# Optimization experiments

Measured on AMD Instinct MI355X. Metric: run time of the kernel, lower is better.

Reference implementation:

```python
import jax, jax.numpy as jnp
import numpy as np

N = 30000      # node_size / new_node_size
R = 1000       # rel_size
T = 300000     # triple_size (edges)
D = 128        # node_hid == rel_hid
B = 1024       # train pairs
NNZ = 600000   # nnz of ent_adj / rel_adj
DEPTH = 2
GAMMA = 3.0
EPS = 1e-12    # F.normalize eps


def setup_inputs():
    key = jax.random.key(0)
    ks = jax.random.split(key, 12)
    adj = jnp.stack([jax.random.randint(ks[0], (T,), 0, N),
                     jax.random.randint(ks[1], (T,), 0, N)]).astype(jnp.int64)
    # one relation per triple: row ids are 0..T-1, col ids are relation ids
    r_index = jnp.stack([jnp.arange(T),
                         jax.random.randint(ks[2], (T,), 0, R)]).astype(jnp.int64)
    r_val = jnp.ones((T,), jnp.float32)
    ent_adj = jnp.stack([jax.random.randint(ks[3], (NNZ,), 0, N),
                         jax.random.randint(ks[4], (NNZ,), 0, N)]).astype(jnp.int64)
    rel_adj = jnp.stack([jax.random.randint(ks[5], (NNZ,), 0, N),
                         jax.random.randint(ks[6], (NNZ,), 0, R)]).astype(jnp.int64)
    ent_emb = jax.random.normal(ks[7], (N, D), jnp.float32) * 0.05
    rel_emb = jax.random.normal(ks[8], (R, D), jnp.float32) * 0.05
    attn_e = jax.random.normal(ks[9], (DEPTH, D, 1), jnp.float32) * 0.1
    attn_r = jax.random.normal(ks[10], (DEPTH, D, 1), jnp.float32) * 0.1
    train_pairs = jax.random.randint(ks[11], (B, 2), 0, N).astype(jnp.int64)
    return dict(ent_emb=ent_emb, rel_emb=rel_emb, attn_e=attn_e, attn_r=attn_r,
                r_val=r_val, adj=adj, r_index=r_index, ent_adj=ent_adj,
                rel_adj=rel_adj, train_pairs=train_pairs)


def _segment_softmax(vals, seg, num):
    m = jax.ops.segment_max(vals, seg, num_segments=num)
    e = jnp.exp(vals - m[seg])
    s = jax.ops.segment_sum(e, seg, num_segments=num)
    return e / s[seg]


def _avg(adj, emb):
    # sparse softmax of an all-ones matrix over dim=1 == 1/deg per nonzero, then spmm
    row, col = adj[0], adj[1]
    deg = jax.ops.segment_sum(jnp.ones_like(row, emb.dtype), row, num_segments=N)
    return jax.ops.segment_sum(emb[col] / deg[row][:, None], row, num_segments=N)


def _gat(features, rel_emb, adj, r_index, r_val, kernels):
    features = jnp.tanh(features)
    outputs = [features]
    row, col = adj[0], adj[1]
    for l in range(DEPTH):
        # sparse [T,R] @ rel_emb  -> per-triple relation embedding
        tri_rel = jax.ops.segment_sum(r_val[:, None] * rel_emb[r_index[1]],
                                      r_index[0], num_segments=T)          # [T,D]
        tri_rel = tri_rel / jnp.maximum(
            jnp.linalg.norm(tri_rel, axis=1, keepdims=True), EPS)
        neighs = features[col]                                             # [T,D]
        neighs = neighs - 2.0 * jnp.sum(neighs * tri_rel, axis=1,
                                        keepdims=True) * tri_rel
        att = jnp.squeeze(tri_rel @ kernels[l], axis=-1)                   # [T]
        att = _segment_softmax(att, row, N)
        new_features = jax.ops.segment_sum(neighs * att[:, None], row,
                                           num_segments=N)
        features = jnp.tanh(new_features)
        outputs.append(features)
    return jnp.concatenate(outputs, axis=-1)  # [N, (DEPTH+1)*D]


def _align_loss(pairs, emb):
    l, r = pairs[:, 0], pairs[:, 1]
    l_emb, r_emb = emb[l], emb[r]
    pos = jnp.sum(jnp.square(l_emb - r_emb), axis=-1, keepdims=True)       # [B,1]

    def sqdist(A, Bm):
        return (jnp.sum(jnp.square(A), axis=1)[:, None]
                + jnp.sum(jnp.square(Bm), axis=1)[None, :]
                - 2.0 * A @ Bm.T)

    bi = jnp.arange(pairs.shape[0])
    mask = jnp.ones((pairs.shape[0], N), emb.dtype)
    mask = mask.at[bi, l].add(-1.0).at[bi, r].add(-1.0)  # 1 - onehot(l) - onehot(r)

    def norm_lse(loss):
        mu = jax.lax.stop_gradient(jnp.mean(loss, axis=-1, keepdims=True))
        sd = jax.lax.stop_gradient(jnp.std(loss, axis=-1, keepdims=True))
        loss = (loss - mu) / sd
        return jax.nn.logsumexp(20.0 * loss + 8.0, axis=-1)

    l_loss = norm_lse((pos - sqdist(l_emb, emb) + GAMMA) * mask)
    r_loss = norm_lse((pos - sqdist(r_emb, emb) + GAMMA) * mask)
    return jnp.mean(l_loss + r_loss)


def reference(ent_emb, rel_emb, attn_e, attn_r, r_val, adj, r_index,
              ent_adj, rel_adj, train_pairs):
    ent_feature = _avg(ent_adj, ent_emb)   # [N,D]
    rel_feature = _avg(rel_adj, rel_emb)   # [N,D]
    out_rel = _gat(rel_feature, rel_emb, adj, r_index, r_val, attn_r)
    out_ent = _gat(ent_feature, rel_emb, adj, r_index, r_val, attn_e)
    emb = jnp.concatenate([out_ent, out_rel], axis=-1)  # [N, 6*D]
    return _align_loss(train_pairs, emb)
```

## Files before the change

### kernel.cpp

```cpp
#include <hip/hip_runtime.h>
#include <math.h>

#define N_ENT 30000
#define R_REL 1000
#define T_EDGE 300000
#define B_PAIR 1024
#define NNZ_E 600000
#define GAMMAF 3.0f
#define EPSV 1e-12f
#define EMBD 768
#define NPAD 30720
#define NT128 240
#define PTILES 480

typedef _Float16 half8 __attribute__((ext_vector_type(8)));
typedef _Float16 half4v __attribute__((ext_vector_type(4)));
typedef _Float16 half2v __attribute__((ext_vector_type(2)));
typedef float f32x4 __attribute__((ext_vector_type(4)));

__device__ inline void gl_lds16(const _Float16* g, _Float16* l){
  __builtin_amdgcn_global_load_lds(
      (const __attribute__((address_space(1))) unsigned int*)g,
      (__attribute__((address_space(3))) unsigned int*)l, 16, 0, 0);
}

__device__ inline float waveRedSum(float v){
  #pragma unroll
  for(int m=32;m>=1;m>>=1) v += __shfl_xor(v, m, 64);
  return v;
}

__device__ inline float fast_tanh(float x){
  x = fminf(10.f, fmaxf(-10.f, x));
  float e = __expf(2.f*x);
  return (e-1.f)/(e+1.f);
}

__global__ __launch_bounds__(256) void k_count3(const int* __restrict__ rA, int* cA,
                                                const int* __restrict__ rE, int* cE,
                                                const int* __restrict__ rR, int* cR){
  int e = blockIdx.x*256 + threadIdx.x;
  if(e < T_EDGE) atomicAdd(&cA[rA[e]], 1);
  if(e < NNZ_E){ atomicAdd(&cE[rE[e]], 1); atomicAdd(&cR[rR[e]], 1); }
}

__global__ __launch_bounds__(1024) void k_scan3(const int* c0, int* s0, int* u0,
                                                const int* c1, int* s1, int* u1,
                                                const int* c2, int* s2, int* u2){
  const int* cnt = blockIdx.x==0 ? c0 : (blockIdx.x==1 ? c1 : c2);
  int* start     = blockIdx.x==0 ? s0 : (blockIdx.x==1 ? s1 : s2);
  int* cursor    = blockIdx.x==0 ? u0 : (blockIdx.x==1 ? u1 : u2);
  __shared__ int wsum[16];
  __shared__ int carry;
  int tid = threadIdx.x, lane = tid & 63, wid = tid >> 6;
  if(tid==0) carry = 0;
  __syncthreads();
  for(int base=0; base<N_ENT; base+=1024){
    int i = base + tid;
    int v = (i<N_ENT)? cnt[i] : 0;
    int x = v;
    #pragma unroll
    for(int off=1; off<64; off<<=1){ int t=__shfl_up(x,off,64); if(lane>=off) x+=t; }
    if(lane==63) wsum[wid]=x;
    __syncthreads();
    if(wid==0){
      int s = (lane<16)? wsum[lane] : 0;
      #pragma unroll
      for(int off=1; off<16; off<<=1){ int t=__shfl_up(s,off,64); if(lane>=off) s+=t; }
      if(lane<16) wsum[lane]=s;
    }
    __syncthreads();
    int wexcl = (wid==0)? 0 : wsum[wid-1];
    int excl = carry + wexcl + x - v;
    if(i<N_ENT){ start[i]=excl; cursor[i]=excl; }
    int tot = wsum[15];
    __syncthreads();
    if(tid==0) carry += tot;
    __syncthreads();
  }
  if(tid==0) start[N_ENT] = carry;
}

__global__ __launch_bounds__(256) void k_scatter3(
      const int* __restrict__ rA, const int* __restrict__ cAj, const int* __restrict__ rid,
      int* uA, int* scolA, int* sridA,
      const int* __restrict__ rE, const int* __restrict__ cEj, int* uE, int* scolE,
      const int* __restrict__ rR, const int* __restrict__ cRj, int* uR, int* scolR){
  int e = blockIdx.x*256 + threadIdx.x;
  if(e < T_EDGE){
    int p = atomicAdd(&uA[rA[e]], 1);
    scolA[p] = cAj[e];
    sridA[p] = rid[e];
  }
  if(e < NNZ_E){
    int p = atomicAdd(&uE[rE[e]], 1);
    scolE[p] = cEj[e];
    int q = atomicAdd(&uR[rR[e]], 1);
    scolR[q] = cRj[e];
  }
}

__global__ __launch_bounds__(256) void k_avg_tanh(const int* __restrict__ start, const int* __restrict__ scol,
                        const float* __restrict__ src, _Float16* featC, _Float16* Eh, int pairOff, int coloff){
  int r = blockIdx.x*4 + (threadIdx.x>>6);
  int lane = threadIdx.x & 63;
  int s0 = start[r], s1 = start[r+1];
  float ax=0.f, ay=0.f;
  int e = s0;
  for(; e+1<s1; e+=2){
    int c0 = scol[e], c1 = scol[e+1];
    float2 v0 = *(const float2*)(src + (size_t)c0*128 + lane*2);
    float2 v1 = *(const float2*)(src + (size_t)c1*128 + lane*2);
    ax += v0.x + v1.x; ay += v0.y + v1.y;
  }
  if(e<s1){
    int c0 = scol[e];
    float2 v0 = *(const float2*)(src + (size_t)c0*128 + lane*2);
    ax += v0.x; ay += v0.y;
  }
  float inv = (s1>s0) ? 1.0f/(float)(s1-s0) : 0.f;
  float vx = fast_tanh(ax*inv), vy = fast_tanh(ay*inv);
  half2v hv = {(_Float16)vx, (_Float16)vy};
  *(half2v*)(featC + (size_t)r*256 + lane*4 + pairOff) = hv;
  *(half2v*)(Eh + (size_t)r*EMBD + coloff + lane*2) = hv;
}

__global__ __launch_bounds__(256) void k_relnorm(const float* __restrict__ rel, const float* __restrict__ ae,
                          const float* __restrict__ ar, _Float16* relnH, float* expdot){
  int r = (blockIdx.x*256 + threadIdx.x) >> 6;
  int lane = threadIdx.x & 63;
  if (r >= R_REL) return;
  float2 v = *(const float2*)(rel + (size_t)r*128 + lane*2);
  float ss = waveRedSum(v.x*v.x + v.y*v.y);
  float nrm = fmaxf(sqrtf(ss), EPSV);
  float2 u; u.x = v.x/nrm; u.y = v.y/nrm;
  half2v uh = {(_Float16)u.x, (_Float16)u.y};
  *(half2v*)(relnH + (size_t)r*128 + lane*2) = uh;
  const float* ks[4] = {ae, ae+128, ar, ar+128};
  #pragma unroll
  for(int k=0;k<4;k++){
    float2 w = *(const float2*)(ks[k] + lane*2);
    float d = waveRedSum(u.x*w.x + u.y*w.y);
    if(lane==0) expdot[k*R_REL + r] = __expf(d);
  }
}

__global__ __launch_bounds__(256) void k_edge2(const int* __restrict__ start, const int* __restrict__ scol,
      const int* __restrict__ srid, const _Float16* __restrict__ relnH,
      const float* __restrict__ expE, const float* __restrict__ expR,
      const _Float16* __restrict__ featIn, _Float16* featOut, _Float16* Eh, int colEnt, int colRel){
  int r = blockIdx.x*4 + (threadIdx.x>>6);
  int lane = threadIdx.x & 63;
  int s0 = start[r], s1 = start[r+1];
  float aEx=0,aEy=0,aRx=0,aRy=0, swE=0, swR=0;
  int e = s0;
  for(; e+1<s1; e+=2){
    int c0=scol[e], q0=srid[e], c1=scol[e+1], q1=srid[e+1];
    float wE0=expE[q0], wR0=expR[q0], wE1=expE[q1], wR1=expR[q1];
    half2v u0h = *(const half2v*)(relnH + (size_t)q0*128 + lane*2);
    half2v u1h = *(const half2v*)(relnH + (size_t)q1*128 + lane*2);
    half4v h0 = *(const half4v*)(featIn + (size_t)c0*256 + lane*4);
    half4v h1 = *(const half4v*)(featIn + (size_t)c1*256 + lane*4);
    float u0x=(float)u0h[0], u0y=(float)u0h[1], u1x=(float)u1h[0], u1y=(float)u1h[1];
    float e0x=(float)h0[0], e0y=(float)h0[1], r0x=(float)h0[2], r0y=(float)h0[3];
    float e1x=(float)h1[0], e1y=(float)h1[1], r1x=(float)h1[2], r1y=(float)h1[3];
    float d0 = e0x*u0x + e0y*u0y;
    float d1 = r0x*u0x + r0y*u0y;
    float d2 = e1x*u1x + e1y*u1y;
    float d3 = r1x*u1x + r1y*u1y;
    #pragma unroll
    for(int m=32;m>=1;m>>=1){
      d0 += __shfl_xor(d0,m,64); d1 += __shfl_xor(d1,m,64);
      d2 += __shfl_xor(d2,m,64); d3 += __shfl_xor(d3,m,64);
    }
    aEx += wE0*(e0x - 2.f*d0*u0x) + wE1*(e1x - 2.f*d2*u1x);
    aEy += wE0*(e0y - 2.f*d0*u0y) + wE1*(e1y - 2.f*d2*u1y);
    aRx += wR0*(r0x - 2.f*d1*u0x) + wR1*(r1x - 2.f*d3*u1x);
    aRy += wR0*(r0y - 2.f*d1*u0y) + wR1*(r1y - 2.f*d3*u1y);
    swE += wE0+wE1; swR += wR0+wR1;
  }
  if(e<s1){
    int c0=scol[e], q0=srid[e];
    float wE0=expE[q0], wR0=expR[q0];
    half2v u0h = *(const half2v*)(relnH + (size_t)q0*128 + lane*2);
    half4v h0 = *(const half4v*)(featIn + (size_t)c0*256 + lane*4);
    float u0x=(float)u0h[0], u0y=(float)u0h[1];
    float e0x=(float)h0[0], e0y=(float)h0[1], r0x=(float)h0[2], r0y=(float)h0[3];
    float d0 = e0x*u0x + e0y*u0y;
    float d1 = r0x*u0x + r0y*u0y;
    #pragma unroll
    for(int m=32;m>=1;m>>=1){ d0 += __shfl_xor(d0,m,64); d1 += __shfl_xor(d1,m,64); }
    aEx += wE0*(e0x - 2.f*d0*u0x);
    aEy += wE0*(e0y - 2.f*d0*u0y);
    aRx += wR0*(r0x - 2.f*d1*u0x);
    aRy += wR0*(r0y - 2.f*d1*u0y);
    swE += wE0; swR += wR0;
  }
  float iE = (s1>s0) ? 1.f/swE : 0.f;
  float iR = (s1>s0) ? 1.f/swR : 0.f;
  float vEx = fast_tanh(aEx*iE), vEy = fast_tanh(aEy*iE);
  float vRx = fast_tanh(aRx*iR), vRy = fast_tanh(aRy*iR);
  half4v ov = {(_Float16)vEx,(_Float16)vEy,(_Float16)vRx,(_Float16)vRy};
  *(half4v*)(featOut + (size_t)r*256 + lane*4) = ov;
  half2v he = {(_Float16)vEx,(_Float16)vEy};
  half2v hr = {(_Float16)vRx,(_Float16)vRy};
  *(half2v*)(Eh + (size_t)r*EMBD + colEnt + lane*2) = he;
  *(half2v*)(Eh + (size_t)r*EMBD + colRel + lane*2) = hr;
}

__global__ __launch_bounds__(256) void k_gather(const _Float16* __restrict__ Eh, const int* __restrict__ tp,
                         _Float16* Wh, float* cvec){
  int i = blockIdx.x; int tid = threadIdx.x;
  int l = tp[2*i], r = tp[2*i+1];
  float sl=0.f, sr=0.f, sp=0.f;
  for(int c=tid;c<EMBD;c+=256){
    _Float16 lh = Eh[(size_t)l*EMBD+c], rh = Eh[(size_t)r*EMBD+c];
    float le = (float)lh, re = (float)rh;
    Wh[(size_t)i*EMBD+c]=lh; Wh[(size_t)(B_PAIR+i)*EMBD+c]=rh;
    sl += le*le; sr += re*re; float d = le-re; sp += d*d;
  }
  __shared__ float s0[256], s1[256], s2[256];
  s0[tid]=sl; s1[tid]=sr; s2[tid]=sp;
  __syncthreads();
  for(int w=128;w>0;w>>=1){
    if(tid<w){ s0[tid]+=s0[tid+w]; s1[tid]+=s1[tid+w]; s2[tid]+=s2[tid+w]; }
    __syncthreads();
  }
  if(tid==0){
    float pos = s2[0];
    cvec[i]        = pos + GAMMAF - s0[0];
    cvec[B_PAIR+i] = pos + GAMMAF - s1[0];
  }
}

__global__ __launch_bounds__(256) void k_qn(const _Float16* __restrict__ Eh, float* qn){
  int j = (blockIdx.x*256 + threadIdx.x) >> 6;
  int lane = threadIdx.x & 63;
  if(j >= NPAD) return;
  if(j >= N_ENT){ if(lane==0) qn[j] = 1e30f; return; }
  float s=0.f;
  #pragma unroll
  for(int q=0;q<12;q++){ float v = (float)Eh[(size_t)j*EMBD + lane + 64*q]; s += v*v; }
  s = waveRedSum(s);
  if(lane==0) qn[j]=s;
}

__global__ __launch_bounds__(256) void k_embstats(const _Float16* __restrict__ Eh, const float* __restrict__ qn,
                           float* Svec, float* Pvec, float* QQ){
  int tid = threadIdx.x;
  int n0 = blockIdx.x*32;
  int nend = n0+32; if(nend > N_ENT) nend = N_ENT;
  float s[3]={0,0,0}, p[3]={0,0,0};
  float q1=0.f, q2=0.f;
  for(int n=n0;n<nend;n++){
    float qv = qn[n];
    if(tid==0){ q1 += qv; q2 += qv*qv; }
    #pragma unroll
    for(int k=0;k<3;k++){
      float v = (float)Eh[(size_t)n*EMBD + tid + k*256];
      s[k] += v; p[k] += qv*v;
    }
  }
  #pragma unroll
  for(int k=0;k<3;k++){
    unsafeAtomicAdd(&Svec[tid + k*256], s[k]);
    unsafeAtomicAdd(&Pvec[tid + k*256], p[k]);
  }
  if(tid==0){ unsafeAtomicAdd(&QQ[0], q1); unsafeAtomicAdd(&QQ[1], q2); }
}

__global__ __launch_bounds__(256) void k_transp(const _Float16* __restrict__ Eh, _Float16* embT){
  __shared__ __align__(16) _Float16 til[64][72];
  int r0 = blockIdx.x*64, c0 = blockIdx.y*64;
  int t = threadIdx.x;
  int rr = t>>3, c8 = (t&7)*8;
  #pragma unroll
  for(int p=0;p<2;p++){
    int gr = r0 + rr + p*32;
    uint4 v = make_uint4(0u,0u,0u,0u);
    if(gr < N_ENT) v = *(const uint4*)(Eh + (size_t)gr*EMBD + c0 + c8);
    *(uint4*)&til[rr + p*32][c8] = v;
  }
  __syncthreads();
  #pragma unroll
  for(int p=0;p<2;p++){
    int cc = rr + p*32;
    __align__(16) _Float16 tmp[8];
    #pragma unroll
    for(int j=0;j<8;j++) tmp[j] = til[c8 + j][cc];
    *(uint4*)(embT + (size_t)(c0+cc)*NPAD + r0 + c8) = *(uint4*)tmp;
  }
}

__global__ __launch_bounds__(256) void k_syrk(const _Float16* __restrict__ embT, float* G){
  __shared__ __align__(16) _Float16 As[128*64];
  __shared__ __align__(16) _Float16 Bs[128*64];
  int tid = threadIdx.x;
  int w = tid>>6, lane = tid&63;
  int quad = lane>>4, l15 = lane&15;
  int lr = lane>>3, lc = lane&7;
  int wm = (w>>1)*64, wn = (w&1)*64;
  int m0 = blockIdx.y*128, n0 = blockIdx.x*128;
  int kbeg = blockIdx.z*3840;
  int kend = kbeg + 3840; if(kend > NPAD) kend = NPAD;
  f32x4 acc[4][4];
  #pragma unroll
  for(int i=0;i<4;i++)
    #pragma unroll
    for(int j=0;j<4;j++) acc[i][j] = (f32x4){0.f,0.f,0.f,0.f};
  for(int k0=kbeg;k0<kend;k0+=64){
    #pragma unroll
    for(int p=0;p<4;p++){
      int r = p*32 + w*8 + lr;
      int cg = lc ^ (r&7);
      gl_lds16(embT + (size_t)(m0+r)*NPAD + k0 + cg*8, As + (p*32 + w*8)*64);
      gl_lds16(embT + (size_t)(n0+r)*NPAD + k0 + cg*8, Bs + (p*32 + w*8)*64);
    }
    __syncthreads();
    #pragma unroll
    for(int ks=0;ks<2;ks++){
      half8 af[4], bf[4];
      #pragma unroll
      for(int i=0;i<4;i++){
        int ml = wm + i*16 + l15;
        af[i] = *(half8*)(As + ml*64 + (((ks<<2)|quad) ^ (ml&7))*8);
      }
      #pragma unroll
      for(int j=0;j<4;j++){
        int nl = wn + j*16 + l15;
        bf[j] = *(half8*)(Bs + nl*64 + (((ks<<2)|quad) ^ (nl&7))*8);
      }
      #pragma unroll
      for(int i=0;i<4;i++)
        #pragma unroll
        for(int j=0;j<4;j++)
          acc[i][j] = __builtin_amdgcn_mfma_f32_16x16x32_f16(af[i], bf[j], acc[i][j], 0,0,0);
    }
    __syncthreads();
  }
  #pragma unroll
  for(int i=0;i<4;i++){
    #pragma unroll
    for(int r=0;r<4;r++){
      int m = m0 + wm + i*16 + quad*4 + r;
      #pragma unroll
      for(int j=0;j<4;j++){
        int n = n0 + wn + j*16 + l15;
        unsafeAtomicAdd(&G[(size_t)m*EMBD + n], acc[i][j][r]);
      }
    }
  }
}

__global__ __launch_bounds__(256) void k_cvtG(const float* __restrict__ G, _Float16* Gh){
  int i = blockIdx.x*256 + threadIdx.x;
  if(i < EMBD*EMBD) Gh[i] = (_Float16)G[i];
}

__device__ inline void mfma_k768(const _Float16* __restrict__ Asrc, const _Float16* __restrict__ Bsrc,
                                 int m0, int n0, int l15, int quad, f32x4 acc[4][4]){
  const _Float16* aB[4]; const _Float16* bB[4];
  #pragma unroll
  for(int i=0;i<4;i++){
    aB[i] = Asrc + (size_t)(m0+i*16+l15)*EMBD + quad*8;
    bB[i] = Bsrc + (size_t)(n0+i*16+l15)*EMBD + quad*8;
  }
  half8 af[2][4], bf[2][4];
  #pragma unroll
  for(int i=0;i<4;i++){ af[0][i] = *(const half8*)(aB[i]); bf[0][i] = *(const half8*)(bB[i]); }
  #pragma unroll
  for(int ks=0; ks<24; ks++){
    int cur = ks&1, nxt = cur^1;
    if(ks<23){
      int ko = (ks+1)*32;
      #pragma unroll
      for(int i=0;i<4;i++){ af[nxt][i] = *(const half8*)(aB[i]+ko); bf[nxt][i] = *(const half8*)(bB[i]+ko); }
    }
    #pragma unroll
    for(int i=0;i<4;i++)
      #pragma unroll
      for(int j=0;j<4;j++)
        acc[i][j] = __builtin_amdgcn_mfma_f32_16x16x32_f16(af[cur][i], bf[cur][j], acc[i][j], 0,0,0);
  }
}

__global__ __launch_bounds__(256) void k_gemmTh(const _Float16* __restrict__ Wh, const _Float16* __restrict__ Gh,
                                                float* Tm){
  int tid = threadIdx.x, w = tid>>6, lane = tid&63;
  int quad = lane>>4, l15 = lane&15;
  int n0 = blockIdx.x*64;
  #pragma unroll
  for(int half=0; half<2; half++){
    int mt = blockIdx.y*8 + half*4 + w;
    int m0 = mt*64;
    f32x4 acc[4][4];
    #pragma unroll
    for(int i=0;i<4;i++)
      #pragma unroll
      for(int j=0;j<4;j++) acc[i][j] = (f32x4){0.f,0.f,0.f,0.f};
    mfma_k768(Wh, Gh, m0, n0, l15, quad, acc);
    #pragma unroll
    for(int i=0;i<4;i++)
      #pragma unroll
      for(int r=0;r<4;r++){
        int mg = m0 + i*16 + quad*4 + r;
        #pragma unroll
        for(int j=0;j<4;j++)
          Tm[(size_t)mg*EMBD + n0 + j*16 + l15] = acc[i][j][r];
      }
  }
}

__global__ __launch_bounds__(256) void k_rowstats(const _Float16* __restrict__ Wh, const float* __restrict__ Tm,
      const _Float16* __restrict__ Eh, const float* __restrict__ qn, const float* __restrict__ cvec,
      const int* __restrict__ tp, const float* __restrict__ Svec, const float* __restrict__ Pvec,
      const float* __restrict__ QQ, float* alpha, float* betav){
  int row = blockIdx.x*4 + (threadIdx.x>>6);
  int lane = threadIdx.x & 63;
  if(row >= 2*B_PAIR) return;
  int pi = row & (B_PAIR-1);
  int lp = tp[2*pi], rp = tp[2*pi+1];
  float d1=0,d2=0,d3=0,dl=0,dr=0;
  #pragma unroll
  for(int k=0;k<12;k++){
    int d = lane + 64*k;
    float a = (float)Wh[(size_t)row*EMBD + d];
    d1 += a*Svec[d];
    d2 += a*Pvec[d];
    d3 += a*Tm[(size_t)row*EMBD + d];
    dl += a*(float)Eh[(size_t)lp*EMBD + d];
    dr += a*(float)Eh[(size_t)rp*EMBD + d];
  }
  d1=waveRedSum(d1); d2=waveRedSum(d2); d3=waveRedSum(d3);
  dl=waveRedSum(dl); dr=waveRedSum(dr);
  if(lane==0){
    double c = (double)cvec[row], Q = (double)QQ[0], Q2 = (double)QQ[1], Nn = (double)N_ENT;
    double su  = Nn*c - Q + 2.0*(double)d1;
    double su2 = Nn*c*c - 2.0*c*Q + Q2 + 4.0*(c*(double)d1 - (double)d2) + 4.0*(double)d3;
    double ul = c - (double)qn[lp] + 2.0*(double)dl;
    double ur = c - (double)qn[rp] + 2.0*(double)dr;
    su -= ul + ur;
    if(lp != rp) su2 -= ul*ul + ur*ur;
    double mu = su/Nn;
    double var = su2/Nn - mu*mu;
    double sd = sqrt(fmax(var, 0.0));
    double al = 20.0/sd;
    alpha[row] = (float)al;
    betav[row] = (float)(8.0 - al*mu);
  }
}

__device__ inline void lseMerge(float& mx, float& sm, float om, float os){
  if(om > mx){ sm = sm*expf(mx-om) + os; mx = om; }
  else if(om != -INFINITY){ sm += os*expf(om-mx); }
}

__global__ __launch_bounds__(256) void k_gemmB(const _Float16* __restrict__ Wh, const _Float16* __restrict__ Eh,
    const float* __restrict__ cvec, const float* __restrict__ qn, const int* __restrict__ tp,
    const float* __restrict__ alpha, const float* __restrict__ betav, float* pm, float* ps){
  __shared__ __align__(16) _Float16 As[128*64];
  __shared__ __align__(16) _Float16 Bs[128*64];
  int id = blockIdx.x;
  int ntile = (id & 7) + ((id >> 7) << 3);
  int m0 = ((id >> 3) & 15) * 128;
  int n0 = ntile * 128;
  int tid = threadIdx.x;
  int w = tid>>6, lane = tid&63;
  int quad = lane>>4, l15 = lane&15;
  int lr = lane>>3, lc = lane&7;
  int wm = (w&1)*64, wn = (w>>1)*64;
  f32x4 acc[4][4];
  #pragma unroll
  for(int i=0;i<4;i++)
    #pragma unroll
    for(int j=0;j<4;j++) acc[i][j] = (f32x4){0.f,0.f,0.f,0.f};
  for(int k0=0;k0<EMBD;k0+=64){
    #pragma unroll
    for(int p=0;p<4;p++){
      int r = p*32 + w*8 + lr;
      int cg = lc ^ (r&7);
      gl_lds16(Wh + (size_t)(m0+r)*EMBD + k0 + cg*8, As + (p*32 + w*8)*64);
      gl_lds16(Eh + (size_t)(n0+r)*EMBD + k0 + cg*8, Bs + (p*32 + w*8)*64);
    }
    __syncthreads();
    #pragma unroll
    for(int ks=0;ks<2;ks++){
      half8 af[4], bf[4];
      #pragma unroll
      for(int i=0;i<4;i++){
        int ml = wm + i*16 + l15;
        af[i] = *(half8*)(As + ml*64 + (((ks<<2)|quad) ^ (ml&7))*8);
      }
      #pragma unroll
      for(int j=0;j<4;j++){
        int nl = wn + j*16 + l15;
        bf[j] = *(half8*)(Bs + nl*64 + (((ks<<2)|quad) ^ (nl&7))*8);
      }
      #pragma unroll
      for(int i=0;i<4;i++)
        #pragma unroll
        for(int j=0;j<4;j++)
          acc[i][j] = __builtin_amdgcn_mfma_f32_16x16x32_f16(af[i], bf[j], acc[i][j], 0,0,0);
    }
    __syncthreads();
  }
  float qv[4]; int jv[4];
  #pragma unroll
  for(int j=0;j<4;j++){ jv[j] = n0 + wn + j*16 + l15; qv[j] = qn[jv[j]]; }
  int ptile = ntile*2 + (w>>1);
  #pragma unroll
  for(int i=0;i<4;i++){
    int mbase = m0 + wm + i*16 + quad*4;
    #pragma unroll
    for(int r=0;r<4;r++){
      int mg = mbase + r;
      int pi = mg & (B_PAIR-1);
      int lp = tp[2*pi], rp = tp[2*pi+1];
      float cv = cvec[mg], al = alpha[mg], be = betav[mg];
      float mx = -INFINITY, sm = 0.f;
      #pragma unroll
      for(int j=0;j<4;j++){
        float u = fmaf(2.f, acc[i][j][r], cv - qv[j]);
        float z = fmaf(al, u, be);
        if(jv[j]==lp || jv[j]==rp) z = (lp==rp) ? fmaf(-al, u, be) : be;
        if(z > mx){ sm = sm*__expf(mx - z) + 1.f; mx = z; }
        else sm += __expf(z - mx);
      }
      #pragma unroll
      for(int m=8;m>=1;m>>=1){
        float om = __shfl_xor(mx, m, 64), os = __shfl_xor(sm, m, 64);
        lseMerge(mx, sm, om, os);
      }
      if(l15==0){ pm[(size_t)mg*PTILES + ptile] = mx; ps[(size_t)mg*PTILES + ptile] = sm; }
    }
  }
}

__global__ __launch_bounds__(256) void k_lse(const float* __restrict__ pm, const float* __restrict__ ps, float* lse){
  __shared__ float shm[256], shs[256];
  int row = blockIdx.x, tid = threadIdx.x;
  float mx = -INFINITY, sm = 0.f;
  for(int t=tid;t<PTILES;t+=256) lseMerge(mx, sm, pm[(size_t)row*PTILES+t], ps[(size_t)row*PTILES+t]);
  shm[tid]=mx; shs[tid]=sm;
  __syncthreads();
  for(int w=128;w>0;w>>=1){
    if(tid<w){
      float m2=shm[tid], s2=shs[tid];
      lseMerge(m2, s2, shm[tid+w], shs[tid+w]);
      shm[tid]=m2; shs[tid]=s2;
    }
    __syncthreads();
  }
  if(tid==0) lse[row] = shm[0] + logf(shs[0]);
}

__global__ __launch_bounds__(256) void k_final(const float* __restrict__ lse, float* out){
  __shared__ double sh[256];
  int tid = threadIdx.x;
  double s = 0.0;
  for(int i=tid;i<B_PAIR;i+=256) s += (double)lse[i] + (double)lse[B_PAIR+i];
  sh[tid]=s; __syncthreads();
  for(int w=128;w>0;w>>=1){ if(tid<w) sh[tid]+=sh[tid+w]; __syncthreads(); }
  if(tid==0) out[0] = (float)(sh[0] / (double)B_PAIR);
}

extern "C" void kernel_launch(void* const* d_in, const int* in_sizes, int n_in,
                              void* d_out, int out_size, void* d_ws, size_t ws_size,
                              hipStream_t stream) {
  const float* ent_emb = (const float*)d_in[0];
  const float* rel_emb = (const float*)d_in[1];
  const float* attn_e  = (const float*)d_in[2];
  const float* attn_r  = (const float*)d_in[3];
  const int* adj     = (const int*)d_in[5];
  const int* r_index = (const int*)d_in[6];
  const int* ent_adj = (const int*)d_in[7];
  const int* rel_adj = (const int*)d_in[8];
  const int* tp      = (const int*)d_in[9];
  float* out = (float*)d_out;

  const int* adj_row = adj;
  const int* adj_col = adj + T_EDGE;
  const int* rid1    = r_index + T_EDGE;

  char* base = (char*)d_ws;
  size_t off = 0;
  auto A = [&](size_t b)->void*{ void* p = base + off; off = (off + b + 255) & ~(size_t)255; return p; };
  int*   cntA  = (int*)  A((size_t)N_ENT*4);
  int*   cntE  = (int*)  A((size_t)N_ENT*4);
  int*   cntR  = (int*)  A((size_t)N_ENT*4);
  float* G     = (float*)A((size_t)EMBD*EMBD*4);
  float* Svec  = (float*)A(EMBD*4);
  float* Pvec  = (float*)A(EMBD*4);
  float* QQ    = (float*)A(2*4);
  size_t zero_end = off;
  int* startA = (int*)A((size_t)(N_ENT+1)*4);
  int* startE = (int*)A((size_t)(N_ENT+1)*4);
  int* startR = (int*)A((size_t)(N_ENT+1)*4);
  int* curA   = (int*)A((size_t)N_ENT*4);
  int* curE   = (int*)A((size_t)N_ENT*4);
  int* curR   = (int*)A((size_t)N_ENT*4);
  int* scolA  = (int*)A((size_t)T_EDGE*4);
  int* sridA  = (int*)A((size_t)T_EDGE*4);
  int* scolE  = (int*)A((size_t)NNZ_E*4);
  int* scolR  = (int*)A((size_t)NNZ_E*4);
  _Float16* Eh = (_Float16*)A((size_t)NPAD*EMBD*2);
  char* X = (char*)A((size_t)EMBD*NPAD*2);
  _Float16* featC0 = (_Float16*)X;
  _Float16* featC1 = (_Float16*)(X + 16u*1024u*1024u);
  _Float16* embT   = (_Float16*)X;
  float*    pm     = (float*)X;
  float*    ps     = (float*)(X + 8u*1024u*1024u);
  _Float16* relnH  = (_Float16*)A((size_t)R_REL*128*2);
  float* expdot  = (float*)A(4*R_REL*4);
  _Float16* Wh   = (_Float16*)A((size_t)2*B_PAIR*EMBD*2);
  _Float16* Gh   = (_Float16*)A((size_t)EMBD*EMBD*2);
  float* Tm      = (float*)A((size_t)2*B_PAIR*EMBD*4);
  float* cvec    = (float*)A(2*B_PAIR*4);
  float* qn      = (float*)A((size_t)NPAD*4);
  float* alpha   = (float*)A(2*B_PAIR*4);
  float* betav   = (float*)A(2*B_PAIR*4);
  float* lse     = (float*)A(2*B_PAIR*4);
  (void)ws_size; (void)in_sizes; (void)n_in; (void)out_size;

  hipMemsetAsync(d_ws, 0, zero_end, stream);
  hipMemsetAsync(Eh + (size_t)N_ENT*EMBD, 0, (size_t)(NPAD-N_ENT)*EMBD*2, stream);

  k_count3<<<(NNZ_E+255)/256, 256, 0, stream>>>(adj_row, cntA, ent_adj, cntE, rel_adj, cntR);
  k_scan3<<<3, 1024, 0, stream>>>(cntA, startA, curA, cntE, startE, curE, cntR, startR, curR);
  k_scatter3<<<(NNZ_E+255)/256, 256, 0, stream>>>(adj_row, adj_col, rid1, curA, scolA, sridA,
                                                  ent_adj, ent_adj+NNZ_E, curE, scolE,
                                                  rel_adj, rel_adj+NNZ_E, curR, scolR);

  k_relnorm<<<R_REL/4, 256, 0, stream>>>(rel_emb, attn_e, attn_r, relnH, expdot);

  k_avg_tanh<<<N_ENT/4, 256, 0, stream>>>(startE, scolE, ent_emb, featC0, Eh, 0, 0);
  k_avg_tanh<<<N_ENT/4, 256, 0, stream>>>(startR, scolR, rel_emb, featC0, Eh, 2, 384);
  k_edge2<<<N_ENT/4, 256, 0, stream>>>(startA, scolA, sridA, relnH, expdot + 0*R_REL, expdot + 2*R_REL,
                                       featC0, featC1, Eh, 128, 512);
  k_edge2<<<N_ENT/4, 256, 0, stream>>>(startA, scolA, sridA, relnH, expdot + 1*R_REL, expdot + 3*R_REL,
                                       featC1, featC0, Eh, 256, 640);

  k_gather<<<B_PAIR, 256, 0, stream>>>(Eh, tp, Wh, cvec);
  k_qn<<<NPAD/4, 256, 0, stream>>>(Eh, qn);
  k_embstats<<<(N_ENT+31)/32, 256, 0, stream>>>(Eh, qn, Svec, Pvec, QQ);
  dim3 gtr(NPAD/64, 12);
  k_transp<<<gtr, 256, 0, stream>>>(Eh, embT);
  dim3 gsy(6, 6, 8);
  k_syrk<<<gsy, 256, 0, stream>>>(embT, G);
  k_cvtG<<<(EMBD*EMBD+255)/256, 256, 0, stream>>>(G, Gh);
  dim3 gT(EMBD/64, 4);
  k_gemmTh<<<gT, 256, 0, stream>>>(Wh, Gh, Tm);
  k_rowstats<<<2*B_PAIR/4, 256, 0, stream>>>(Wh, Tm, Eh, qn, cvec, tp, Svec, Pvec, QQ, alpha, betav);
  k_gemmB<<<NT128*16, 256, 0, stream>>>(Wh, Eh, cvec, qn, tp, alpha, betav, pm, ps);
  k_lse<<<2*B_PAIR, 256, 0, stream>>>(pm, ps, lse);
  k_final<<<1, 256, 0, stream>>>(lse, out);
}
```

Measured before the change: 949.4 us.

## Fuse small kernels, cache fp16 embeddings, and merge loss reduction stages

Several small launches are merged into fewer kernels. A new prep kernel converts entity and relation embeddings to fp16, zeroes the Eh padding and computes the relation norms. The two averaging passes become one 2D launch that gathers fp16 rows. qn and the embedding statistics are computed in a single persistent pass. The G fp16 conversion now happens on the fly inside gemmTh, and the final mean is folded into the lse kernel with an atomic counter. gemmB also gets an occupancy hint. The aim is to cut launch overhead and gather bandwidth, at the cost of fp16 rounding of the inputs before averaging and an order-dependent float atomic sum for the loss.

```diff
diff --git a/kernel.cpp b/kernel.cpp
--- a/kernel.cpp
+++ b/kernel.cpp
@@ -100,8 +100,43 @@
   }
 }
 
-__global__ __launch_bounds__(256) void k_avg_tanh(const int* __restrict__ start, const int* __restrict__ scol,
-                        const float* __restrict__ src, _Float16* featC, _Float16* Eh, int pairOff, int coloff){
+__global__ __launch_bounds__(256) void k_prep(const float* __restrict__ ent, const float* __restrict__ rel,
+      const float* __restrict__ ae, const float* __restrict__ ar,
+      _Float16* ehE, _Float16* ehR, _Float16* Eh, _Float16* relnH, float* expdot){
+  int i = blockIdx.x*256 + threadIdx.x;
+  if(i < N_ENT*128) ehE[i] = (_Float16)ent[i];
+  if(i < R_REL*128) ehR[i] = (_Float16)rel[i];
+  if(i < (NPAD-N_ENT)*EMBD) Eh[(size_t)N_ENT*EMBD + i] = (_Float16)0.f;
+  int r = i >> 6;
+  if(r < R_REL){
+    int lane = i & 63;
+    float2 v = *(const float2*)(rel + (size_t)r*128 + lane*2);
+    float ss = waveRedSum(v.x*v.x + v.y*v.y);
+    float nrm = fmaxf(sqrtf(ss), EPSV);
+    float2 u; u.x = v.x/nrm; u.y = v.y/nrm;
+    half2v uh = {(_Float16)u.x, (_Float16)u.y};
+    *(half2v*)(relnH + (size_t)r*128 + lane*2) = uh;
+    const float* ks[4] = {ae, ae+128, ar, ar+128};
+    #pragma unroll
+    for(int k=0;k<4;k++){
+      float2 w = *(const float2*)(ks[k] + lane*2);
+      float d = waveRedSum(u.x*w.x + u.y*w.y);
+      if(lane==0) expdot[k*R_REL + r] = __expf(d);
+    }
+  }
+}
+
+__global__ __launch_bounds__(256) void k_avg2(const int* __restrict__ startE, const int* __restrict__ scolE,
+                        const _Float16* __restrict__ srcE,
+                        const int* __restrict__ startR, const int* __restrict__ scolR,
+                        const _Float16* __restrict__ srcR,
+                        _Float16* featC, _Float16* Eh){
+  int which = blockIdx.y;
+  const int* start = which? startR : startE;
+  const int* scol  = which? scolR : scolE;
+  const _Float16* src = which? srcR : srcE;
+  int pairOff = which? 2 : 0;
+  int coloff  = which? 384 : 0;
   int r = blockIdx.x*4 + (threadIdx.x>>6);
   int lane = threadIdx.x & 63;
   int s0 = start[r], s1 = start[r+1];
@@ -109,40 +144,20 @@
   int e = s0;
   for(; e+1<s1; e+=2){
     int c0 = scol[e], c1 = scol[e+1];
-    float2 v0 = *(const float2*)(src + (size_t)c0*128 + lane*2);
-    float2 v1 = *(const float2*)(src + (size_t)c1*128 + lane*2);
-    ax += v0.x + v1.x; ay += v0.y + v1.y;
+    half2v v0 = *(const half2v*)(src + (size_t)c0*128 + lane*2);
+    half2v v1 = *(const half2v*)(src + (size_t)c1*128 + lane*2);
+    ax += (float)v0[0] + (float)v1[0]; ay += (float)v0[1] + (float)v1[1];
   }
   if(e<s1){
     int c0 = scol[e];
-    float2 v0 = *(const float2*)(src + (size_t)c0*128 + lane*2);
-    ax += v0.x; ay += v0.y;
+    half2v v0 = *(const half2v*)(src + (size_t)c0*128 + lane*2);
+    ax += (float)v0[0]; ay += (float)v0[1];
   }
   float inv = (s1>s0) ? 1.0f/(float)(s1-s0) : 0.f;
   float vx = fast_tanh(ax*inv), vy = fast_tanh(ay*inv);
   half2v hv = {(_Float16)vx, (_Float16)vy};
   *(half2v*)(featC + (size_t)r*256 + lane*4 + pairOff) = hv;
   *(half2v*)(Eh + (size_t)r*EMBD + coloff + lane*2) = hv;
-}
-
-__global__ __launch_bounds__(256) void k_relnorm(const float* __restrict__ rel, const float* __restrict__ ae,
-                          const float* __restrict__ ar, _Float16* relnH, float* expdot){
-  int r = (blockIdx.x*256 + threadIdx.x) >> 6;
-  int lane = threadIdx.x & 63;
-  if (r >= R_REL) return;
-  float2 v = *(const float2*)(rel + (size_t)r*128 + lane*2);
-  float ss = waveRedSum(v.x*v.x + v.y*v.y);
-  float nrm = fmaxf(sqrtf(ss), EPSV);
-  float2 u; u.x = v.x/nrm; u.y = v.y/nrm;
-  half2v uh = {(_Float16)u.x, (_Float16)u.y};
-  *(half2v*)(relnH + (size_t)r*128 + lane*2) = uh;
-  const float* ks[4] = {ae, ae+128, ar, ar+128};
-  #pragma unroll
-  for(int k=0;k<4;k++){
-    float2 w = *(const float2*)(ks[k] + lane*2);
-    float d = waveRedSum(u.x*w.x + u.y*w.y);
-    if(lane==0) expdot[k*R_REL + r] = __expf(d);
-  }
 }
 
 __global__ __launch_bounds__(256) void k_edge2(const int* __restrict__ start, const int* __restrict__ scol,
@@ -233,40 +248,30 @@
   }
 }
 
-__global__ __launch_bounds__(256) void k_qn(const _Float16* __restrict__ Eh, float* qn){
-  int j = (blockIdx.x*256 + threadIdx.x) >> 6;
-  int lane = threadIdx.x & 63;
-  if(j >= NPAD) return;
-  if(j >= N_ENT){ if(lane==0) qn[j] = 1e30f; return; }
-  float s=0.f;
-  #pragma unroll
-  for(int q=0;q<12;q++){ float v = (float)Eh[(size_t)j*EMBD + lane + 64*q]; s += v*v; }
-  s = waveRedSum(s);
-  if(lane==0) qn[j]=s;
-}
-
-__global__ __launch_bounds__(256) void k_embstats(const _Float16* __restrict__ Eh, const float* __restrict__ qn,
+__global__ __launch_bounds__(256) void k_qnstats(const _Float16* __restrict__ Eh, float* qn,
                            float* Svec, float* Pvec, float* QQ){
-  int tid = threadIdx.x;
-  int n0 = blockIdx.x*32;
-  int nend = n0+32; if(nend > N_ENT) nend = N_ENT;
-  float s[3]={0,0,0}, p[3]={0,0,0};
+  int wid = threadIdx.x>>6, lane = threadIdx.x&63;
+  int gw = blockIdx.x*4 + wid;
+  float s[12], p[12];
+  #pragma unroll
+  for(int q=0;q<12;q++){ s[q]=0.f; p[q]=0.f; }
   float q1=0.f, q2=0.f;
-  for(int n=n0;n<nend;n++){
-    float qv = qn[n];
-    if(tid==0){ q1 += qv; q2 += qv*qv; }
-    #pragma unroll
-    for(int k=0;k<3;k++){
-      float v = (float)Eh[(size_t)n*EMBD + tid + k*256];
-      s[k] += v; p[k] += qv*v;
-    }
-  }
-  #pragma unroll
-  for(int k=0;k<3;k++){
-    unsafeAtomicAdd(&Svec[tid + k*256], s[k]);
-    unsafeAtomicAdd(&Pvec[tid + k*256], p[k]);
-  }
-  if(tid==0){ unsafeAtomicAdd(&QQ[0], q1); unsafeAtomicAdd(&QQ[1], q2); }
+  for(int r=gw; r<NPAD; r+=960){
+    if(r >= N_ENT){ if(lane==0) qn[r] = 1e30f; continue; }
+    float v[12]; float ss=0.f;
+    #pragma unroll
+    for(int q=0;q<12;q++){ v[q] = (float)Eh[(size_t)r*EMBD + lane + 64*q]; ss += v[q]*v[q]; }
+    ss = waveRedSum(ss);
+    if(lane==0){ qn[r] = ss; q1 += ss; q2 += ss*ss; }
+    #pragma unroll
+    for(int q=0;q<12;q++){ s[q] += v[q]; p[q] += ss*v[q]; }
+  }
+  #pragma unroll
+  for(int q=0;q<12;q++){
+    unsafeAtomicAdd(&Svec[lane + 64*q], s[q]);
+    unsafeAtomicAdd(&Pvec[lane + 64*q], p[q]);
+  }
+  if(lane==0){ unsafeAtomicAdd(&QQ[0], q1); unsafeAtomicAdd(&QQ[1], q2); }
 }
 
 __global__ __launch_bounds__(256) void k_transp(const _Float16* __restrict__ Eh, _Float16* embT){
@@ -352,53 +357,43 @@
   }
 }
 
-__global__ __launch_bounds__(256) void k_cvtG(const float* __restrict__ G, _Float16* Gh){
-  int i = blockIdx.x*256 + threadIdx.x;
-  if(i < EMBD*EMBD) Gh[i] = (_Float16)G[i];
-}
-
-__device__ inline void mfma_k768(const _Float16* __restrict__ Asrc, const _Float16* __restrict__ Bsrc,
-                                 int m0, int n0, int l15, int quad, f32x4 acc[4][4]){
-  const _Float16* aB[4]; const _Float16* bB[4];
-  #pragma unroll
-  for(int i=0;i<4;i++){
-    aB[i] = Asrc + (size_t)(m0+i*16+l15)*EMBD + quad*8;
-    bB[i] = Bsrc + (size_t)(n0+i*16+l15)*EMBD + quad*8;
-  }
-  half8 af[2][4], bf[2][4];
-  #pragma unroll
-  for(int i=0;i<4;i++){ af[0][i] = *(const half8*)(aB[i]); bf[0][i] = *(const half8*)(bB[i]); }
-  #pragma unroll
-  for(int ks=0; ks<24; ks++){
-    int cur = ks&1, nxt = cur^1;
-    if(ks<23){
-      int ko = (ks+1)*32;
-      #pragma unroll
-      for(int i=0;i<4;i++){ af[nxt][i] = *(const half8*)(aB[i]+ko); bf[nxt][i] = *(const half8*)(bB[i]+ko); }
-    }
-    #pragma unroll
-    for(int i=0;i<4;i++)
-      #pragma unroll
-      for(int j=0;j<4;j++)
-        acc[i][j] = __builtin_amdgcn_mfma_f32_16x16x32_f16(af[cur][i], bf[cur][j], acc[i][j], 0,0,0);
-  }
-}
-
-__global__ __launch_bounds__(256) void k_gemmTh(const _Float16* __restrict__ Wh, const _Float16* __restrict__ Gh,
+__global__ __launch_bounds__(256) void k_gemmTh(const _Float16* __restrict__ Wh, const float* __restrict__ G,
                                                 float* Tm){
   int tid = threadIdx.x, w = tid>>6, lane = tid&63;
   int quad = lane>>4, l15 = lane&15;
   int n0 = blockIdx.x*64;
   #pragma unroll
   for(int half=0; half<2; half++){
-    int mt = blockIdx.y*8 + half*4 + w;
-    int m0 = mt*64;
+    int m0 = (blockIdx.y*8 + half*4 + w)*64;
     f32x4 acc[4][4];
     #pragma unroll
     for(int i=0;i<4;i++)
       #pragma unroll
       for(int j=0;j<4;j++) acc[i][j] = (f32x4){0.f,0.f,0.f,0.f};
-    mfma_k768(Wh, Gh, m0, n0, l15, quad, acc);
+    const _Float16* aB[4]; const float* bB[4];
+    #pragma unroll
+    for(int i=0;i<4;i++){
+      aB[i] = Wh + (size_t)(m0+i*16+l15)*EMBD + quad*8;
+      bB[i] = G  + (size_t)(n0+i*16+l15)*EMBD + quad*8;
+    }
+    for(int ks=0; ks<24; ks++){
+      half8 af[4], bf[4];
+      #pragma unroll
+      for(int i=0;i<4;i++) af[i] = *(const half8*)(aB[i] + ks*32);
+      #pragma unroll
+      for(int j=0;j<4;j++){
+        float4 f0 = *(const float4*)(bB[j] + ks*32);
+        float4 f1 = *(const float4*)(bB[j] + ks*32 + 4);
+        half8 h = {(_Float16)f0.x,(_Float16)f0.y,(_Float16)f0.z,(_Float16)f0.w,
+                   (_Float16)f1.x,(_Float16)f1.y,(_Float16)f1.z,(_Float16)f1.w};
+        bf[j] = h;
+      }
+      #pragma unroll
+      for(int i=0;i<4;i++)
+        #pragma unroll
+        for(int j=0;j<4;j++)
+          acc[i][j] = __builtin_amdgcn_mfma_f32_16x16x32_f16(af[i], bf[j], acc[i][j], 0,0,0);
+    }
     #pragma unroll
     for(int i=0;i<4;i++)
       #pragma unroll
@@ -455,7 +450,7 @@
   else if(om != -INFINITY){ sm += os*expf(om-mx); }
 }
 
-__global__ __launch_bounds__(256) void k_gemmB(const _Float16* __restrict__ Wh, const _Float16* __restrict__ Eh,
+__global__ __launch_bounds__(256,3) void k_gemmB(const _Float16* __restrict__ Wh, const _Float16* __restrict__ Eh,
     const float* __restrict__ cvec, const float* __restrict__ qn, const int* __restrict__ tp,
     const float* __restrict__ alpha, const float* __restrict__ betav, float* pm, float* ps){
   __shared__ __align__(16) _Float16 As[128*64];
@@ -536,7 +531,8 @@
   }
 }
 
-__global__ __launch_bounds__(256) void k_lse(const float* __restrict__ pm, const float* __restrict__ ps, float* lse){
+__global__ __launch_bounds__(256) void k_lse2(const float* __restrict__ pm, const float* __restrict__ ps,
+                        float* accum, int* done, float* out){
   __shared__ float shm[256], shs[256];
   int row = blockIdx.x, tid = threadIdx.x;
   float mx = -INFINITY, sm = 0.f;
@@ -551,17 +547,17 @@
     }
     __syncthreads();
   }
-  if(tid==0) lse[row] = shm[0] + logf(shs[0]);
-}
-
-__global__ __launch_bounds__(256) void k_final(const float* __restrict__ lse, float* out){
-  __shared__ double sh[256];
-  int tid = threadIdx.x;
-  double s = 0.0;
-  for(int i=tid;i<B_PAIR;i+=256) s += (double)lse[i] + (double)lse[B_PAIR+i];
-  sh[tid]=s; __syncthreads();
-  for(int w=128;w>0;w>>=1){ if(tid<w) sh[tid]+=sh[tid+w]; __syncthreads(); }
-  if(tid==0) out[0] = (float)(sh[0] / (double)B_PAIR);
+  if(tid==0){
+    float l = shm[0] + logf(shs[0]);
+    atomicAdd(accum, l);
+    __threadfence();
+    int t = atomicAdd(done, 1);
+    if(t == 2*B_PAIR - 1){
+      __threadfence();
+      float total = atomicAdd(accum, 0.0f);
+      out[0] = total / (float)B_PAIR;
+    }
+  }
 }
 
 extern "C" void kernel_launch(void* const* d_in, const int* in_sizes, int n_in,
@@ -592,6 +588,8 @@
   float* Svec  = (float*)A(EMBD*4);
   float* Pvec  = (float*)A(EMBD*4);
   float* QQ    = (float*)A(2*4);
+  float* accum = (float*)A(4);
+  int*   done  = (int*)  A(4);
   size_t zero_end = off;
   int* startA = (int*)A((size_t)(N_ENT+1)*4);
   int* startE = (int*)A((size_t)(N_ENT+1)*4);
@@ -611,19 +609,18 @@
   float*    pm     = (float*)X;
   float*    ps     = (float*)(X + 8u*1024u*1024u);
   _Float16* relnH  = (_Float16*)A((size_t)R_REL*128*2);
+  _Float16* ehE   = (_Float16*)A((size_t)N_ENT*128*2);
+  _Float16* ehR   = (_Float16*)A((size_t)R_REL*128*2);
   float* expdot  = (float*)A(4*R_REL*4);
   _Float16* Wh   = (_Float16*)A((size_t)2*B_PAIR*EMBD*2);
-  _Float16* Gh   = (_Float16*)A((size_t)EMBD*EMBD*2);
   float* Tm      = (float*)A((size_t)2*B_PAIR*EMBD*4);
   float* cvec    = (float*)A(2*B_PAIR*4);
   float* qn      = (float*)A((size_t)NPAD*4);
   float* alpha   = (float*)A(2*B_PAIR*4);
   float* betav   = (float*)A(2*B_PAIR*4);
-  float* lse     = (float*)A(2*B_PAIR*4);
   (void)ws_size; (void)in_sizes; (void)n_in; (void)out_size;
 
   hipMemsetAsync(d_ws, 0, zero_end, stream);
-  hipMemsetAsync(Eh + (size_t)N_ENT*EMBD, 0, (size_t)(NPAD-N_ENT)*EMBD*2, stream);
 
   k_count3<<<(NNZ_E+255)/256, 256, 0, stream>>>(adj_row, cntA, ent_adj, cntE, rel_adj, cntR);
   k_scan3<<<3, 1024, 0, stream>>>(cntA, startA, curA, cntE, startE, curE, cntR, startR, curR);
@@ -631,27 +628,25 @@
                                                   ent_adj, ent_adj+NNZ_E, curE, scolE,
                                                   rel_adj, rel_adj+NNZ_E, curR, scolR);
 
-  k_relnorm<<<R_REL/4, 256, 0, stream>>>(rel_emb, attn_e, attn_r, relnH, expdot);
-
-  k_avg_tanh<<<N_ENT/4, 256, 0, stream>>>(startE, scolE, ent_emb, featC0, Eh, 0, 0);
-  k_avg_tanh<<<N_ENT/4, 256, 0, stream>>>(startR, scolR, rel_emb, featC0, Eh, 2, 384);
+  k_prep<<<(N_ENT*128+255)/256, 256, 0, stream>>>(ent_emb, rel_emb, attn_e, attn_r,
+                                                  ehE, ehR, Eh, relnH, expdot);
+
+  dim3 gavg(N_ENT/4, 2);
+  k_avg2<<<gavg, 256, 0, stream>>>(startE, scolE, ehE, startR, scolR, ehR, featC0, Eh);
   k_edge2<<<N_ENT/4, 256, 0, stream>>>(startA, scolA, sridA, relnH, expdot + 0*R_REL, expdot + 2*R_REL,
                                        featC0, featC1, Eh, 128, 512);
   k_edge2<<<N_ENT/4, 256, 0, stream>>>(startA, scolA, sridA, relnH, expdot + 1*R_REL, expdot + 3*R_REL,
                                        featC1, featC0, Eh, 256, 640);
 
   k_gather<<<B_PAIR, 256, 0, stream>>>(Eh, tp, Wh, cvec);
-  k_qn<<<NPAD/4, 256, 0, stream>>>(Eh, qn);
-  k_embstats<<<(N_ENT+31)/32, 256, 0, stream>>>(Eh, qn, Svec, Pvec, QQ);
+  k_qnstats<<<240, 256, 0, stream>>>(Eh, qn, Svec, Pvec, QQ);
   dim3 gtr(NPAD/64, 12);
   k_transp<<<gtr, 256, 0, stream>>>(Eh, embT);
   dim3 gsy(6, 6, 8);
   k_syrk<<<gsy, 256, 0, stream>>>(embT, G);
-  k_cvtG<<<(EMBD*EMBD+255)/256, 256, 0, stream>>>(G, Gh);
   dim3 gT(EMBD/64, 4);
-  k_gemmTh<<<gT, 256, 0, stream>>>(Wh, Gh, Tm);
+  k_gemmTh<<<gT, 256, 0, stream>>>(Wh, G, Tm);
   k_rowstats<<<2*B_PAIR/4, 256, 0, stream>>>(Wh, Tm, Eh, qn, cvec, tp, Svec, Pvec, QQ, alpha, betav);
   k_gemmB<<<NT128*16, 256, 0, stream>>>(Wh, Eh, cvec, qn, tp, alpha, betav, pm, ps);
-  k_lse<<<2*B_PAIR, 256, 0, stream>>>(pm, ps, lse);
-  k_final<<<1, 256, 0, stream>>>(lse, out);
-}
+  k_lse2<<<2*B_PAIR, 256, 0, stream>>>(pm, ps, accum, done, out);
+}
```

New measurement: 889.4 us. -6.3%, faster.
